# Kernel tuning notes

Hardware: AMD Instinct MI355X
Metric: run time of the kernel (lower is better)

Reference implementation:

```python
import jax, jax.numpy as jnp
import numpy as np

B, N, CA, CS, CZ, H, NQ, NK = 2, 16384, 128, 128, 16, 4, 32, 128
DH = CA // H
NB = N // NQ


def _ln(x, gamma=None, eps=1e-5):
    m = jnp.mean(x, -1, keepdims=True)
    v = jnp.var(x, -1, keepdims=True)
    y = (x - m) * jax.lax.rsqrt(v + eps)
    return y if gamma is None else y * gamma


def _adaln(a, s, gamma_s, Wg, bg, Wskip):
    # AF3 Algorithm 26: LN(a) without affine; LN(s) with scale, no offset;
    # out = sigmoid(Linear(s)) * a + LinearNoBias(s)
    a_n = _ln(a)
    s_n = _ln(s, gamma_s)
    return jax.nn.sigmoid(s_n @ Wg + bg) * a_n + s_n @ Wskip


def setup_inputs():
    key = jax.random.key(0)
    ks = jax.random.split(key, 20)
    def nrm(i, shape, scale=0.02):
        return jax.random.normal(ks[i], shape, jnp.float32) * scale
    return {
        "a": jax.random.normal(ks[0], (B, N, CA), jnp.float32),
        "s": jax.random.normal(ks[1], (B, N, CS), jnp.float32),
        "z": jax.random.normal(ks[2], (B, NB, NQ, NK, CZ), jnp.float32),
        "apb_gamma_s": jnp.ones((CS,), jnp.float32),
        "apb_Wg": nrm(3, (CS, CA)),
        "apb_bg": jnp.zeros((CA,), jnp.float32),
        "apb_Wskip": nrm(4, (CS, CA)),
        "Wq": nrm(5, (CA, CA)), "bq": jnp.zeros((CA,), jnp.float32),
        "Wk": nrm(6, (CA, CA)), "Wv": nrm(7, (CA, CA)),
        "Wgate": nrm(8, (CA, CA)), "Wo": nrm(9, (CA, CA)),
        "gamma_z": jnp.ones((CZ,), jnp.float32),
        "Wz": nrm(10, (CZ, H)),
        "Ws_last": nrm(11, (CS, CA)),
        "bs_last": jnp.full((CA,), -2.0, jnp.float32),
        "ct_gamma_s": jnp.ones((CS,), jnp.float32),
        "ct_Wg": nrm(12, (CS, CA)), "ct_bg": jnp.zeros((CA,), jnp.float32),
        "ct_Wskip": nrm(13, (CS, CA)),
        "Wa1": nrm(14, (CA, 2 * CA)), "Wa2": nrm(15, (CA, 2 * CA)),
        "Wb": nrm(16, (2 * CA, CA)),
        "Ws": nrm(17, (CS, CA)), "bs": jnp.full((CA,), -2.0, jnp.float32),
        "n_queries": NQ, "n_keys": NK,
    }


def reference(a, s, z, apb_gamma_s, apb_Wg, apb_bg, apb_Wskip, Wq, bq, Wk, Wv,
              Wgate, Wo, gamma_z, Wz, Ws_last, bs_last, ct_gamma_s, ct_Wg,
              ct_bg, ct_Wskip, Wa1, Wa2, Wb, Ws, bs, n_queries, n_keys):
    nq, nk = int(n_queries), int(n_keys)
    nb = N // nq
    # ---- AttentionPairBias, local windowed attention ----
    a1 = _adaln(a, s, apb_gamma_s, apb_Wg, apb_bg, apb_Wskip)  # [B,N,CA]
    # trunked pair bias: [B,nb,nq,nk,H] -> [B,H,nb,nq,nk]
    bias = jnp.transpose(_ln(z, gamma_z) @ Wz, (0, 4, 1, 2, 3))
    q = (a1 @ Wq + bq).reshape(B, N, H, DH).transpose(0, 2, 1, 3)
    k = (a1 @ Wk).reshape(B, N, H, DH).transpose(0, 2, 1, 3)
    v = (a1 @ Wv).reshape(B, N, H, DH).transpose(0, 2, 1, 3)
    qb = q.reshape(B, H, nb, nq, DH)
    pad = (nk - nq) // 2
    # centered key window per query block
    idx = (jnp.arange(nb) * nq - pad)[:, None] + jnp.arange(nk)[None, :]  # [nb,nk]
    valid = (idx >= 0) & (idx < N)
    idxc = jnp.clip(idx, 0, N - 1)
    kb = k[:, :, idxc]  # [B,H,nb,nk,DH]
    vb = v[:, :, idxc]
    scores = jnp.einsum('bhnqd,bhnkd->bhnqk', qb, kb) / np.sqrt(DH).astype(np.float32) + bias
    scores = jnp.where(valid[None, None, :, None, :], scores, -1e9)
    attn = jax.nn.softmax(scores, axis=-1)
    o = jnp.einsum('bhnqk,bhnkd->bhnqd', attn, vb)  # [B,H,nb,nq,DH]
    o = o.reshape(B, H, N, DH).transpose(0, 2, 1, 3).reshape(B, N, CA)
    g = jax.nn.sigmoid(a1 @ Wgate)  # per-channel gating
    attn_out = (g * o) @ Wo
    b_out = jax.nn.sigmoid(s @ Ws_last + bs_last) * attn_out
    # ---- ConditionedTransitionBlock (Alg 25) ----
    a3 = _adaln(a, s, ct_gamma_s, ct_Wg, ct_bg, ct_Wskip)
    t = jax.nn.silu(a3 @ Wa1) * (a3 @ Wa2)
    ct_out = jax.nn.sigmoid(s @ Ws + bs) * (t @ Wb)
    # Alg 23: a = b + ConditionedTransitionBlock(a, s)
    return b_out + ct_out
```

## Files before the change

kernel.cpp:

```cpp
#include <hip/hip_runtime.h>

typedef _Float16 f16;
typedef f16 f16x8 __attribute__((ext_vector_type(8)));
typedef f16 f16x4 __attribute__((ext_vector_type(4)));
typedef f16 f16x2 __attribute__((ext_vector_type(2)));
typedef float f32x4 __attribute__((ext_vector_type(4)));

#define MFMA16(a,b,c) __builtin_amdgcn_mfma_f32_16x16x32_f16((a),(b),(c),0,0,0)

static __device__ __forceinline__ f16x8 ld8(const f16* p){ return *(const f16x8*)p; }
static __device__ __forceinline__ float sigm(float x){ return 1.f/(1.f + __expf(-x)); }

__global__ __launch_bounds__(256) void k_prep(
    const float* __restrict__ apb_gamma, const float* __restrict__ apb_Wg, const float* __restrict__ apb_Wskip,
    const float* __restrict__ ct_gamma,  const float* __restrict__ ct_Wg,  const float* __restrict__ ct_Wskip,
    const float* __restrict__ Wq, const float* __restrict__ Wk, const float* __restrict__ Wv, const float* __restrict__ Wgate,
    const float* __restrict__ Wsl, const float* __restrict__ Wss,
    const float* __restrict__ Wa1, const float* __restrict__ Wa2,
    const float* __restrict__ Wo, const float* __restrict__ Wb,
    const float* __restrict__ gamma_z, const float* __restrict__ Wz,
    f16* __restrict__ wA, f16* __restrict__ wC, f16* __restrict__ wQK, f16* __restrict__ wVG,
    f16* __restrict__ wSG, f16* __restrict__ wAB, f16* __restrict__ wO, f16* __restrict__ wBt,
    float* __restrict__ wzg)
{
  const int t0 = blockIdx.x*256 + threadIdx.x;
  const int stride = gridDim.x*256;
  for (int i = t0; i < 256*128; i += stride){
    const int n = i >> 7, k = i & 127;
    const int m = n & 127;
    wA[i]  = (f16)(((n<128) ? apb_Wg[k*128+m] : apb_Wskip[k*128+m]) * apb_gamma[k]);
    wC[i]  = (f16)(((n<128) ? ct_Wg[k*128+m]  : ct_Wskip[k*128+m])  * ct_gamma[k]);
    wQK[i] = (f16)((n<128) ? Wq[k*128+m] : Wk[k*128+m]);
    wVG[i] = (f16)((n<128) ? Wv[k*128+m] : Wgate[k*128+m]);
    wSG[i] = (f16)((n<128) ? Wsl[k*128+m] : Wss[k*128+m]);
  }
  for (int i = t0; i < 512*128; i += stride){
    const int n = i >> 7, k = i & 127;
    wAB[i] = (f16)((n & 1) ? Wa2[k*256 + (n>>1)] : Wa1[k*256 + (n>>1)]);
  }
  for (int i = t0; i < 128*128; i += stride){
    const int n = i >> 7, k = i & 127;
    wO[i] = (f16)Wo[k*128+n];
  }
  for (int i = t0; i < 128*256; i += stride){
    const int n = i >> 8, k = i & 255;
    wBt[i] = (f16)Wb[k*128+n];
  }
  if (t0 < 64) wzg[t0] = gamma_z[t0 & 15] * Wz[(t0 & 15)*4 + (t0 >> 4)];
}

__global__ __launch_bounds__(256) void k_ln(const float* __restrict__ A, const float* __restrict__ S,
    f16* __restrict__ An, f16* __restrict__ Sn, f16* __restrict__ Sh)
{
  const int w = threadIdx.x >> 6, l = threadIdx.x & 63;
  const size_t row = (size_t)blockIdx.x*4 + w;
  const float2 av = *(const float2*)(A + row*128 + l*2);
  const float2 sv = *(const float2*)(S + row*128 + l*2);
  float sa = av.x + av.y, qa = av.x*av.x + av.y*av.y;
  float ss = sv.x + sv.y, qs = sv.x*sv.x + sv.y*sv.y;
  #pragma unroll
  for (int o = 32; o; o >>= 1){
    sa += __shfl_xor(sa, o); qa += __shfl_xor(qa, o);
    ss += __shfl_xor(ss, o); qs += __shfl_xor(qs, o);
  }
  const float ma = sa*(1.f/128.f), va = qa*(1.f/128.f) - ma*ma;
  const float ms = ss*(1.f/128.f), vs = qs*(1.f/128.f) - ms*ms;
  const float ra = rsqrtf(va + 1e-5f), rs = rsqrtf(vs + 1e-5f);
  f16x2 o1; o1[0] = (f16)((av.x-ma)*ra); o1[1] = (f16)((av.y-ma)*ra);
  *(f16x2*)(An + row*128 + l*2) = o1;
  f16x2 o2; o2[0] = (f16)((sv.x-ms)*rs); o2[1] = (f16)((sv.y-ms)*rs);
  *(f16x2*)(Sn + row*128 + l*2) = o2;
  f16x2 o3; o3[0] = (f16)sv.x; o3[1] = (f16)sv.y;
  *(f16x2*)(Sh + row*128 + l*2) = o3;
}

template<int MODE>
__global__ __launch_bounds__(256) void k_gemm256(
    const f16* __restrict__ X, const f16* __restrict__ Wt,
    const float* __restrict__ bias0, const float* __restrict__ bias1,
    const f16* __restrict__ aux, f16* __restrict__ out0, f16* __restrict__ out1)
{
  const int l = threadIdx.x & 63, w = threadIdx.x >> 6;
  const int c = l & 15, q4 = l >> 4;
  const int n0 = blockIdx.y * 16;
  f16x8 b0[4], b1[4];
  #pragma unroll
  for (int kc = 0; kc < 4; kc++){
    b0[kc] = ld8(Wt + (size_t)(n0 + c)*128 + kc*32 + q4*8);
    b1[kc] = ld8(Wt + (size_t)(128 + n0 + c)*128 + kc*32 + q4*8);
  }
  float bv0 = 0.f, bv1 = 0.f;
  if (MODE == 0 || MODE == 1 || MODE == 2) bv0 = bias0[n0 + c];
  if (MODE == 1) bv1 = bias1[n0 + c];

  for (int mi = 0; mi < 4; mi++){
    const int mbase = blockIdx.x*256 + w*64 + mi*16;
    const f16* xp = X + (size_t)(mbase + c)*128 + q4*8;
    f32x4 d0 = {0.f,0.f,0.f,0.f}, d1 = {0.f,0.f,0.f,0.f};
    #pragma unroll
    for (int kc = 0; kc < 4; kc++){
      f16x8 av = ld8(xp + kc*32);
      d0 = MFMA16(av, b0[kc], d0);
      d1 = MFMA16(av, b1[kc], d1);
    }
    if (MODE == 0){
      #pragma unroll
      for (int r = 0; r < 4; r++){
        const size_t row = mbase + q4*4 + r;
        const float anv = (float)aux[row*128 + n0 + c];
        out0[row*128 + n0 + c] = (f16)(sigm(d0[r] + bv0)*anv + d1[r]);
      }
    } else if (MODE == 1){
      #pragma unroll
      for (int r = 0; r < 4; r++){
        const size_t row = mbase + q4*4 + r;
        out0[row*128 + n0 + c] = (f16)sigm(d0[r] + bv0);
        out1[row*128 + n0 + c] = (f16)sigm(d1[r] + bv1);
      }
    } else if (MODE == 2){
      #pragma unroll
      for (int r = 0; r < 4; r++){
        const size_t row = mbase + q4*4 + r;
        out0[row*128 + n0 + c] = (f16)((d0[r] + bv0)*0.17677669529663687f);
        out1[row*128 + n0 + c] = (f16)d1[r];
      }
    } else {
      f16x4 vv;
      #pragma unroll
      for (int r = 0; r < 4; r++) vv[r] = (f16)d0[r];
      const int bidx = mbase >> 14;
      const int ntk  = (mbase & 16383) + q4*4;
      *(f16x4*)(out0 + ((size_t)bidx*128 + n0 + c)*16384 + ntk) = vv;
      #pragma unroll
      for (int r = 0; r < 4; r++){
        const size_t row = mbase + q4*4 + r;
        out1[row*128 + n0 + c] = (f16)sigm(d1[r]);
      }
    }
  }
}

__global__ __launch_bounds__(256) void k_ab(const f16* __restrict__ X, const f16* __restrict__ Wt,
                                            f16* __restrict__ T)
{
  const int l = threadIdx.x & 63, w = threadIdx.x >> 6;
  const int c = l & 15, q4 = l >> 4;
  const int n0 = blockIdx.y * 32;
  f16x8 b0[4], b1[4];
  #pragma unroll
  for (int kc = 0; kc < 4; kc++){
    b0[kc] = ld8(Wt + (size_t)(n0 + c)*128 + kc*32 + q4*8);
    b1[kc] = ld8(Wt + (size_t)(n0 + 16 + c)*128 + kc*32 + q4*8);
  }
  for (int mi = 0; mi < 4; mi++){
    const int mbase = blockIdx.x*256 + w*64 + mi*16;
    const f16* xp = X + (size_t)(mbase + c)*128 + q4*8;
    f32x4 d0 = {0.f,0.f,0.f,0.f}, d1 = {0.f,0.f,0.f,0.f};
    #pragma unroll
    for (int kc = 0; kc < 4; kc++){
      f16x8 av = ld8(xp + kc*32);
      d0 = MFMA16(av, b0[kc], d0);
      d1 = MFMA16(av, b1[kc], d1);
    }
    #pragma unroll
    for (int tile = 0; tile < 2; tile++){
      #pragma unroll
      for (int r = 0; r < 4; r++){
        const float dv = tile ? d1[r] : d0[r];
        const float ov = __shfl_xor(dv, 1);
        const float u  = (c & 1) ? ov : dv;
        const float vv = (c & 1) ? dv : ov;
        const float tvv = (u * sigm(u)) * vv;
        if (!(c & 1)){
          const size_t row = mbase + q4*4 + r;
          T[row*256 + ((n0 + tile*16 + c) >> 1)] = (f16)tvv;
        }
      }
    }
  }
}

__global__ __launch_bounds__(512) void k_attn(const f16* __restrict__ Q, const f16* __restrict__ K,
    const f16* __restrict__ VT, const float* __restrict__ Z, const float* __restrict__ WZG,
    f16* __restrict__ Og)
{
  __shared__ f16 kl[128*136];
  __shared__ f16 vtl[128*136];
  __shared__ f16 upb[17408];
  __shared__ float wzg_s[64];
  const int tid = threadIdx.x;
  const int b = blockIdx.x >> 9, nb = blockIdx.x & 511;
  if (tid < 64) wzg_s[tid] = WZG[tid];
  {
    const int j = tid >> 2, seg = tid & 3;
    const long kt = (long)nb*32 - 48 + j;
    const f16* ks = K + ((long)b*16384 + kt)*128 + seg*32;
    *(f16x8*)&kl[j*136 + seg*32]      = ld8(ks);
    *(f16x8*)&kl[j*136 + seg*32 + 8]  = ld8(ks + 8);
    *(f16x8*)&kl[j*136 + seg*32 + 16] = ld8(ks + 16);
    *(f16x8*)&kl[j*136 + seg*32 + 24] = ld8(ks + 24);
    const f16* vs = VT + ((long)b*128 + j)*16384 + (long)nb*32 - 48 + seg*32;
    *(f16x8*)&vtl[j*136 + seg*32]      = ld8(vs);
    *(f16x8*)&vtl[j*136 + seg*32 + 8]  = ld8(vs + 8);
    *(f16x8*)&vtl[j*136 + seg*32 + 16] = ld8(vs + 16);
    *(f16x8*)&vtl[j*136 + seg*32 + 24] = ld8(vs + 24);
  }
  __syncthreads();
  #pragma unroll
  for (int i = 0; i < 8; i++){
    const int p  = tid + i*512;
    const int qq = p >> 7, kk = p & 127;
    const float* zp = Z + ((((size_t)b*512 + nb)*32 + qq)*128 + kk)*16;
    const float4 z0 = *(const float4*)(zp);
    const float4 z1 = *(const float4*)(zp + 4);
    const float4 z2 = *(const float4*)(zp + 8);
    const float4 z3 = *(const float4*)(zp + 12);
    const float xs[16] = {z0.x,z0.y,z0.z,z0.w, z1.x,z1.y,z1.z,z1.w,
                          z2.x,z2.y,z2.z,z2.w, z3.x,z3.y,z3.z,z3.w};
    float sm = 0.f, sq = 0.f;
    #pragma unroll
    for (int cc = 0; cc < 16; cc++){ sm += xs[cc]; sq += xs[cc]*xs[cc]; }
    const float mean = sm*(1.f/16.f);
    const float var  = sq*(1.f/16.f) - mean*mean;
    const float rs   = rsqrtf(var + 1e-5f);
    #pragma unroll
    for (int h = 0; h < 4; h++){
      float acc = 0.f;
      #pragma unroll
      for (int cc = 0; cc < 16; cc++) acc += (xs[cc]-mean)*wzg_s[h*16+cc];
      upb[(h*32 + qq)*132 + kk] = (f16)(acc*rs);
    }
  }
  __syncthreads();

  const int l = tid & 63, w = tid >> 6;
  const int c = l & 15, q4 = l >> 4;
  const int h = w >> 1, qh = w & 1, m0 = qh*16;
  const f16x8 aq = ld8(Q + ((size_t)b*16384 + (size_t)nb*32 + m0 + c)*128 + h*32 + q4*8);
  f32x4 sc[8];
  #pragma unroll
  for (int nt = 0; nt < 8; nt++){
    const f16x8 bf = *(const f16x8*)&kl[(nt*16 + c)*136 + h*32 + q4*8];
    f32x4 zz = {0.f,0.f,0.f,0.f};
    sc[nt] = MFMA16(aq, bf, zz);
  }
  #pragma unroll
  for (int nt = 0; nt < 8; nt++){
    const int key = nt*16 + c;
    const long kt = (long)nb*32 - 48 + key;
    const bool inv = (kt < 0) || (kt >= 16384);
    #pragma unroll
    for (int r = 0; r < 4; r++){
      const float v = sc[nt][r] + (float)upb[(h*32 + m0 + q4*4 + r)*132 + key];
      sc[nt][r] = inv ? -1e9f : v;
    }
  }
  #pragma unroll
  for (int r = 0; r < 4; r++){
    float mx = sc[0][r];
    #pragma unroll
    for (int nt = 1; nt < 8; nt++) mx = fmaxf(mx, sc[nt][r]);
    #pragma unroll
    for (int o = 8; o; o >>= 1) mx = fmaxf(mx, __shfl_xor(mx, o));
    float sum = 0.f;
    #pragma unroll
    for (int nt = 0; nt < 8; nt++){ const float e = __expf(sc[nt][r]-mx); sc[nt][r] = e; sum += e; }
    #pragma unroll
    for (int o = 8; o; o >>= 1) sum += __shfl_xor(sum, o);
    const float inv = 1.f/sum;
    #pragma unroll
    for (int nt = 0; nt < 8; nt++) sc[nt][r] *= inv;
  }
  __syncthreads();
  #pragma unroll
  for (int nt = 0; nt < 8; nt++)
    #pragma unroll
    for (int r = 0; r < 4; r++)
      upb[(w*16 + q4*4 + r)*136 + nt*16 + c] = (f16)sc[nt][r];
  f32x4 o0 = {0.f,0.f,0.f,0.f}, o1 = {0.f,0.f,0.f,0.f};
  #pragma unroll
  for (int kc = 0; kc < 4; kc++){
    const f16x8 pa = *(const f16x8*)&upb[(w*16 + c)*136 + kc*32 + q4*8];
    const f16x8 v0 = *(const f16x8*)&vtl[(h*32 + c)*136 + kc*32 + q4*8];
    const f16x8 v1 = *(const f16x8*)&vtl[(h*32 + 16 + c)*136 + kc*32 + q4*8];
    o0 = MFMA16(pa, v0, o0);
    o1 = MFMA16(pa, v1, o1);
  }
  #pragma unroll
  for (int r = 0; r < 4; r++){
    const size_t tok = (size_t)b*16384 + (size_t)nb*32 + m0 + q4*4 + r;
    Og[tok*128 + h*32 + c]      = (f16)o0[r];
    Og[tok*128 + h*32 + 16 + c] = (f16)o1[r];
  }
}

__global__ __launch_bounds__(256) void k_final(const f16* __restrict__ G, const f16* __restrict__ O,
    const f16* __restrict__ T, const f16* __restrict__ Wot, const f16* __restrict__ Wbt,
    const f16* __restrict__ GL, const f16* __restrict__ GS, float* __restrict__ out)
{
  const int l = threadIdx.x & 63, w = threadIdx.x >> 6;
  const int c = l & 15, q4 = l >> 4;
  #pragma unroll
  for (int nt = 0; nt < 2; nt++){
    const int cb = blockIdx.y*32 + nt*16;
    f16x8 bo[4], bb[8];
    #pragma unroll
    for (int kc = 0; kc < 4; kc++) bo[kc] = ld8(Wot + (size_t)(cb + c)*128 + kc*32 + q4*8);
    #pragma unroll
    for (int kc = 0; kc < 8; kc++) bb[kc] = ld8(Wbt + (size_t)(cb + c)*256 + kc*32 + q4*8);
    for (int mi = 0; mi < 4; mi++){
      const int mbase = blockIdx.x*256 + w*64 + mi*16;
      f32x4 d1 = {0.f,0.f,0.f,0.f}, d2 = {0.f,0.f,0.f,0.f};
      const f16* gp = G + (size_t)(mbase + c)*128 + q4*8;
      const f16* op = O + (size_t)(mbase + c)*128 + q4*8;
      #pragma unroll
      for (int kc = 0; kc < 4; kc++){
        const f16x8 av = ld8(gp + kc*32) * ld8(op + kc*32);
        d1 = MFMA16(av, bo[kc], d1);
      }
      const f16* tp = T + (size_t)(mbase + c)*256 + q4*8;
      #pragma unroll
      for (int kc = 0; kc < 8; kc++) d2 = MFMA16(ld8(tp + kc*32), bb[kc], d2);
      #pragma unroll
      for (int r = 0; r < 4; r++){
        const size_t row = mbase + q4*4 + r;
        const float glv = (float)GL[row*128 + cb + c];
        const float gsv = (float)GS[row*128 + cb + c];
        out[row*128 + cb + c] = glv*d1[r] + gsv*d2[r];
      }
    }
  }
}

extern "C" void kernel_launch(void* const* d_in, const int* in_sizes, int n_in,
                              void* d_out, int out_size, void* d_ws, size_t ws_size,
                              hipStream_t stream)
{
  (void)in_sizes; (void)n_in; (void)out_size; (void)ws_size;
  const float* a        = (const float*)d_in[0];
  const float* s        = (const float*)d_in[1];
  const float* z        = (const float*)d_in[2];
  const float* apb_gamma= (const float*)d_in[3];
  const float* apb_Wg   = (const float*)d_in[4];
  const float* apb_bg   = (const float*)d_in[5];
  const float* apb_Wskip= (const float*)d_in[6];
  const float* Wq       = (const float*)d_in[7];
  const float* bq       = (const float*)d_in[8];
  const float* Wk       = (const float*)d_in[9];
  const float* Wv       = (const float*)d_in[10];
  const float* Wgate    = (const float*)d_in[11];
  const float* Wo       = (const float*)d_in[12];
  const float* gamma_z  = (const float*)d_in[13];
  const float* Wz       = (const float*)d_in[14];
  const float* Wsl      = (const float*)d_in[15];
  const float* bsl      = (const float*)d_in[16];
  const float* ct_gamma = (const float*)d_in[17];
  const float* ct_Wg    = (const float*)d_in[18];
  const float* ct_bg    = (const float*)d_in[19];
  const float* ct_Wskip = (const float*)d_in[20];
  const float* Wa1      = (const float*)d_in[21];
  const float* Wa2      = (const float*)d_in[22];
  const float* Wb       = (const float*)d_in[23];
  const float* Wss      = (const float*)d_in[24];
  const float* bss      = (const float*)d_in[25];

  f16* W0 = (f16*)d_ws;
  const size_t SL = (size_t)32768*128;
  f16* an = W0 + 0*SL;   f16* qv = an;
  f16* sn = W0 + 1*SL;   f16* kv = sn;
  f16* sh = W0 + 2*SL;   f16* vt = sh;
  f16* a1 = W0 + 3*SL;   f16* ov = a1;
  f16* a3 = W0 + 4*SL;
  f16* gl = W0 + 5*SL;
  f16* gs = W0 + 6*SL;
  f16* gv = W0 + 7*SL;
  f16* tv = W0 + 8*SL;
  f16* wA  = W0 + 10*SL;
  f16* wC  = wA  + 256*128;
  f16* wQK = wC  + 256*128;
  f16* wVG = wQK + 256*128;
  f16* wSG = wVG + 256*128;
  f16* wAB = wSG + 256*128;
  f16* wO  = wAB + 512*128;
  f16* wBt = wO  + 128*128;
  float* wzg = (float*)(wBt + 128*256);

  k_prep<<<dim3(64),256,0,stream>>>(apb_gamma,apb_Wg,apb_Wskip, ct_gamma,ct_Wg,ct_Wskip,
      Wq,Wk,Wv,Wgate, Wsl,Wss, Wa1,Wa2, Wo,Wb, gamma_z,Wz,
      wA,wC,wQK,wVG,wSG,wAB,wO,wBt,wzg);
  k_ln<<<dim3(8192),256,0,stream>>>(a,s,an,sn,sh);
  k_gemm256<0><<<dim3(128,8),256,0,stream>>>(sn,wA,apb_bg,nullptr,an,a1,nullptr);
  k_gemm256<0><<<dim3(128,8),256,0,stream>>>(sn,wC,ct_bg,nullptr,an,a3,nullptr);
  k_gemm256<1><<<dim3(128,8),256,0,stream>>>(sh,wSG,bsl,bss,nullptr,gl,gs);
  k_gemm256<2><<<dim3(128,8),256,0,stream>>>(a1,wQK,bq,nullptr,nullptr,qv,kv);
  k_gemm256<3><<<dim3(128,8),256,0,stream>>>(a1,wVG,nullptr,nullptr,nullptr,vt,gv);
  k_ab<<<dim3(128,16),256,0,stream>>>(a3,wAB,tv);
  k_attn<<<dim3(1024),512,0,stream>>>(qv,kv,vt,z,wzg,ov);
  k_final<<<dim3(128,4),256,0,stream>>>(gv,ov,tv,wO,wBt,gl,gs,(float*)d_out);
}
```

Baseline: 610.5 us.

## Fuse paired projection GEMMs and read K/V directly from global in attention

```diff
diff --git a/kernel.cpp b/kernel.cpp
--- a/kernel.cpp
+++ b/kernel.cpp
@@ -74,11 +74,50 @@
   *(f16x2*)(Sh + row*128 + l*2) = o3;
 }
 
-template<int MODE>
-__global__ __launch_bounds__(256) void k_gemm256(
+__global__ __launch_bounds__(256) void k_adaln(
+    const f16* __restrict__ Sn, const f16* __restrict__ An,
+    const f16* __restrict__ wA, const f16* __restrict__ wC,
+    const float* __restrict__ bgA, const float* __restrict__ bgC,
+    f16* __restrict__ A1, f16* __restrict__ A3)
+{
+  const int l = threadIdx.x & 63, w = threadIdx.x >> 6;
+  const int c = l & 15, q4 = l >> 4;
+  const int n0 = blockIdx.y * 16;
+  f16x8 bA0[4], bA1[4], bC0[4], bC1[4];
+  #pragma unroll
+  for (int kc = 0; kc < 4; kc++){
+    bA0[kc] = ld8(wA + (size_t)(n0 + c)*128 + kc*32 + q4*8);
+    bA1[kc] = ld8(wA + (size_t)(128 + n0 + c)*128 + kc*32 + q4*8);
+    bC0[kc] = ld8(wC + (size_t)(n0 + c)*128 + kc*32 + q4*8);
+    bC1[kc] = ld8(wC + (size_t)(128 + n0 + c)*128 + kc*32 + q4*8);
+  }
+  const float bvA = bgA[n0 + c], bvC = bgC[n0 + c];
+  for (int mi = 0; mi < 4; mi++){
+    const int mbase = blockIdx.x*256 + w*64 + mi*16;
+    const f16* xp = Sn + (size_t)(mbase + c)*128 + q4*8;
+    f32x4 dA0 = {0,0,0,0}, dA1 = {0,0,0,0}, dC0 = {0,0,0,0}, dC1 = {0,0,0,0};
+    #pragma unroll
+    for (int kc = 0; kc < 4; kc++){
+      f16x8 av = ld8(xp + kc*32);
+      dA0 = MFMA16(av, bA0[kc], dA0);
+      dA1 = MFMA16(av, bA1[kc], dA1);
+      dC0 = MFMA16(av, bC0[kc], dC0);
+      dC1 = MFMA16(av, bC1[kc], dC1);
+    }
+    #pragma unroll
+    for (int r = 0; r < 4; r++){
+      const size_t row = mbase + q4*4 + r;
+      const float anv = (float)An[row*128 + n0 + c];
+      A1[row*128 + n0 + c] = (f16)(sigm(dA0[r] + bvA)*anv + dA1[r]);
+      A3[row*128 + n0 + c] = (f16)(sigm(dC0[r] + bvC)*anv + dC1[r]);
+    }
+  }
+}
+
+__global__ __launch_bounds__(256) void k_gates(
     const f16* __restrict__ X, const f16* __restrict__ Wt,
     const float* __restrict__ bias0, const float* __restrict__ bias1,
-    const f16* __restrict__ aux, f16* __restrict__ out0, f16* __restrict__ out1)
+    f16* __restrict__ out0, f16* __restrict__ out1)
 {
   const int l = threadIdx.x & 63, w = threadIdx.x >> 6;
   const int c = l & 15, q4 = l >> 4;
@@ -89,54 +128,68 @@
     b0[kc] = ld8(Wt + (size_t)(n0 + c)*128 + kc*32 + q4*8);
     b1[kc] = ld8(Wt + (size_t)(128 + n0 + c)*128 + kc*32 + q4*8);
   }
-  float bv0 = 0.f, bv1 = 0.f;
-  if (MODE == 0 || MODE == 1 || MODE == 2) bv0 = bias0[n0 + c];
-  if (MODE == 1) bv1 = bias1[n0 + c];
-
+  const float bv0 = bias0[n0 + c], bv1 = bias1[n0 + c];
   for (int mi = 0; mi < 4; mi++){
     const int mbase = blockIdx.x*256 + w*64 + mi*16;
     const f16* xp = X + (size_t)(mbase + c)*128 + q4*8;
-    f32x4 d0 = {0.f,0.f,0.f,0.f}, d1 = {0.f,0.f,0.f,0.f};
+    f32x4 d0 = {0,0,0,0}, d1 = {0,0,0,0};
     #pragma unroll
     for (int kc = 0; kc < 4; kc++){
       f16x8 av = ld8(xp + kc*32);
       d0 = MFMA16(av, b0[kc], d0);
       d1 = MFMA16(av, b1[kc], d1);
     }
-    if (MODE == 0){
-      #pragma unroll
-      for (int r = 0; r < 4; r++){
-        const size_t row = mbase + q4*4 + r;
-        const float anv = (float)aux[row*128 + n0 + c];
-        out0[row*128 + n0 + c] = (f16)(sigm(d0[r] + bv0)*anv + d1[r]);
-      }
-    } else if (MODE == 1){
-      #pragma unroll
-      for (int r = 0; r < 4; r++){
-        const size_t row = mbase + q4*4 + r;
-        out0[row*128 + n0 + c] = (f16)sigm(d0[r] + bv0);
-        out1[row*128 + n0 + c] = (f16)sigm(d1[r] + bv1);
-      }
-    } else if (MODE == 2){
-      #pragma unroll
-      for (int r = 0; r < 4; r++){
-        const size_t row = mbase + q4*4 + r;
-        out0[row*128 + n0 + c] = (f16)((d0[r] + bv0)*0.17677669529663687f);
-        out1[row*128 + n0 + c] = (f16)d1[r];
-      }
-    } else {
-      f16x4 vv;
-      #pragma unroll
-      for (int r = 0; r < 4; r++) vv[r] = (f16)d0[r];
-      const int bidx = mbase >> 14;
-      const int ntk  = (mbase & 16383) + q4*4;
-      *(f16x4*)(out0 + ((size_t)bidx*128 + n0 + c)*16384 + ntk) = vv;
-      #pragma unroll
-      for (int r = 0; r < 4; r++){
-        const size_t row = mbase + q4*4 + r;
-        out1[row*128 + n0 + c] = (f16)sigm(d1[r]);
-      }
-    }
+    #pragma unroll
+    for (int r = 0; r < 4; r++){
+      const size_t row = mbase + q4*4 + r;
+      out0[row*128 + n0 + c] = (f16)sigm(d0[r] + bv0);
+      out1[row*128 + n0 + c] = (f16)sigm(d1[r] + bv1);
+    }
+  }
+}
+
+__global__ __launch_bounds__(256) void k_qkvg(
+    const f16* __restrict__ X, const f16* __restrict__ wQK, const f16* __restrict__ wVG,
+    const float* __restrict__ bq,
+    f16* __restrict__ Qo, f16* __restrict__ Ko, f16* __restrict__ Vt, f16* __restrict__ Go)
+{
+  const int l = threadIdx.x & 63, w = threadIdx.x >> 6;
+  const int c = l & 15, q4 = l >> 4;
+  const int n0 = blockIdx.y * 16;
+  f16x8 bQ[4], bK[4], bV[4], bG[4];
+  #pragma unroll
+  for (int kc = 0; kc < 4; kc++){
+    bQ[kc] = ld8(wQK + (size_t)(n0 + c)*128 + kc*32 + q4*8);
+    bK[kc] = ld8(wQK + (size_t)(128 + n0 + c)*128 + kc*32 + q4*8);
+    bV[kc] = ld8(wVG + (size_t)(n0 + c)*128 + kc*32 + q4*8);
+    bG[kc] = ld8(wVG + (size_t)(128 + n0 + c)*128 + kc*32 + q4*8);
+  }
+  const float bvq = bq[n0 + c];
+  for (int mi = 0; mi < 4; mi++){
+    const int mbase = blockIdx.x*256 + w*64 + mi*16;
+    const f16* xp = X + (size_t)(mbase + c)*128 + q4*8;
+    f32x4 dQ = {0,0,0,0}, dK = {0,0,0,0}, dV = {0,0,0,0}, dG = {0,0,0,0};
+    #pragma unroll
+    for (int kc = 0; kc < 4; kc++){
+      f16x8 av = ld8(xp + kc*32);
+      dQ = MFMA16(av, bQ[kc], dQ);
+      dK = MFMA16(av, bK[kc], dK);
+      dV = MFMA16(av, bV[kc], dV);
+      dG = MFMA16(av, bG[kc], dG);
+    }
+    #pragma unroll
+    for (int r = 0; r < 4; r++){
+      const size_t row = mbase + q4*4 + r;
+      Qo[row*128 + n0 + c] = (f16)((dQ[r] + bvq)*0.17677669529663687f);
+      Ko[row*128 + n0 + c] = (f16)dK[r];
+      Go[row*128 + n0 + c] = (f16)sigm(dG[r]);
+    }
+    f16x4 vv;
+    #pragma unroll
+    for (int r = 0; r < 4; r++) vv[r] = (f16)dV[r];
+    const int bidx = mbase >> 14;
+    const int ntk  = (mbase & 16383) + q4*4;
+    *(f16x4*)(Vt + ((size_t)bidx*128 + n0 + c)*16384 + ntk) = vv;
   }
 }
 
@@ -155,7 +208,7 @@
   for (int mi = 0; mi < 4; mi++){
     const int mbase = blockIdx.x*256 + w*64 + mi*16;
     const f16* xp = X + (size_t)(mbase + c)*128 + q4*8;
-    f32x4 d0 = {0.f,0.f,0.f,0.f}, d1 = {0.f,0.f,0.f,0.f};
+    f32x4 d0 = {0,0,0,0}, d1 = {0,0,0,0};
     #pragma unroll
     for (int kc = 0; kc < 4; kc++){
       f16x8 av = ld8(xp + kc*32);
@@ -184,27 +237,11 @@
     const f16* __restrict__ VT, const float* __restrict__ Z, const float* __restrict__ WZG,
     f16* __restrict__ Og)
 {
-  __shared__ f16 kl[128*136];
-  __shared__ f16 vtl[128*136];
   __shared__ f16 upb[17408];
   __shared__ float wzg_s[64];
   const int tid = threadIdx.x;
   const int b = blockIdx.x >> 9, nb = blockIdx.x & 511;
   if (tid < 64) wzg_s[tid] = WZG[tid];
-  {
-    const int j = tid >> 2, seg = tid & 3;
-    const long kt = (long)nb*32 - 48 + j;
-    const f16* ks = K + ((long)b*16384 + kt)*128 + seg*32;
-    *(f16x8*)&kl[j*136 + seg*32]      = ld8(ks);
-    *(f16x8*)&kl[j*136 + seg*32 + 8]  = ld8(ks + 8);
-    *(f16x8*)&kl[j*136 + seg*32 + 16] = ld8(ks + 16);
-    *(f16x8*)&kl[j*136 + seg*32 + 24] = ld8(ks + 24);
-    const f16* vs = VT + ((long)b*128 + j)*16384 + (long)nb*32 - 48 + seg*32;
-    *(f16x8*)&vtl[j*136 + seg*32]      = ld8(vs);
-    *(f16x8*)&vtl[j*136 + seg*32 + 8]  = ld8(vs + 8);
-    *(f16x8*)&vtl[j*136 + seg*32 + 16] = ld8(vs + 16);
-    *(f16x8*)&vtl[j*136 + seg*32 + 24] = ld8(vs + 24);
-  }
   __syncthreads();
   #pragma unroll
   for (int i = 0; i < 8; i++){
@@ -237,10 +274,11 @@
   const int c = l & 15, q4 = l >> 4;
   const int h = w >> 1, qh = w & 1, m0 = qh*16;
   const f16x8 aq = ld8(Q + ((size_t)b*16384 + (size_t)nb*32 + m0 + c)*128 + h*32 + q4*8);
+  const long kbase = (long)b*16384 + (long)nb*32 - 48;
   f32x4 sc[8];
   #pragma unroll
   for (int nt = 0; nt < 8; nt++){
-    const f16x8 bf = *(const f16x8*)&kl[(nt*16 + c)*136 + h*32 + q4*8];
+    const f16x8 bf = ld8(K + (kbase + nt*16 + c)*128 + h*32 + q4*8);
     f32x4 zz = {0.f,0.f,0.f,0.f};
     sc[nt] = MFMA16(aq, bf, zz);
   }
@@ -277,12 +315,13 @@
     #pragma unroll
     for (int r = 0; r < 4; r++)
       upb[(w*16 + q4*4 + r)*136 + nt*16 + c] = (f16)sc[nt][r];
+  const f16* vb = VT + ((long)b*128)*16384 + (long)nb*32 - 48;
   f32x4 o0 = {0.f,0.f,0.f,0.f}, o1 = {0.f,0.f,0.f,0.f};
   #pragma unroll
   for (int kc = 0; kc < 4; kc++){
     const f16x8 pa = *(const f16x8*)&upb[(w*16 + c)*136 + kc*32 + q4*8];
-    const f16x8 v0 = *(const f16x8*)&vtl[(h*32 + c)*136 + kc*32 + q4*8];
-    const f16x8 v1 = *(const f16x8*)&vtl[(h*32 + 16 + c)*136 + kc*32 + q4*8];
+    const f16x8 v0 = ld8(vb + (long)(h*32 + c)*16384 + kc*32 + q4*8);
+    const f16x8 v1 = ld8(vb + (long)(h*32 + 16 + c)*16384 + kc*32 + q4*8);
     o0 = MFMA16(pa, v0, o0);
     o1 = MFMA16(pa, v1, o1);
   }
@@ -389,11 +428,9 @@
       Wq,Wk,Wv,Wgate, Wsl,Wss, Wa1,Wa2, Wo,Wb, gamma_z,Wz,
       wA,wC,wQK,wVG,wSG,wAB,wO,wBt,wzg);
   k_ln<<<dim3(8192),256,0,stream>>>(a,s,an,sn,sh);
-  k_gemm256<0><<<dim3(128,8),256,0,stream>>>(sn,wA,apb_bg,nullptr,an,a1,nullptr);
-  k_gemm256<0><<<dim3(128,8),256,0,stream>>>(sn,wC,ct_bg,nullptr,an,a3,nullptr);
-  k_gemm256<1><<<dim3(128,8),256,0,stream>>>(sh,wSG,bsl,bss,nullptr,gl,gs);
-  k_gemm256<2><<<dim3(128,8),256,0,stream>>>(a1,wQK,bq,nullptr,nullptr,qv,kv);
-  k_gemm256<3><<<dim3(128,8),256,0,stream>>>(a1,wVG,nullptr,nullptr,nullptr,vt,gv);
+  k_adaln<<<dim3(128,8),256,0,stream>>>(sn,an,wA,wC,apb_bg,ct_bg,a1,a3);
+  k_gates<<<dim3(128,8),256,0,stream>>>(sh,wSG,bsl,bss,gl,gs);
+  k_qkvg<<<dim3(128,8),256,0,stream>>>(a1,wQK,wVG,bq,qv,kv,vt,gv);
   k_ab<<<dim3(128,16),256,0,stream>>>(a3,wAB,tv);
   k_attn<<<dim3(1024),512,0,stream>>>(qv,kv,vt,z,wzg,ov);
   k_final<<<dim3(128,4),256,0,stream>>>(gv,ov,tv,wO,wBt,gl,gs,(float*)d_out);
```

Result: no change. 602.4 us (-1.3%).
